# Performance work log

Measured on AMD Instinct MI355X. Metric: run time of the kernel, lower is better.

## Reference

```python
import jax, jax.numpy as jnp
import numpy as np

COORD_W, WIDTH_W, CLASS_W, P0_W = 5.0, 2.0, 1.0, 2.0
BETA = 0.1  # SmoothL1 beta
PEN_W = jnp.array([0.1, 1.0, 1.0], jnp.float32)  # CE class weights


def _lsa(C):
    """Jonker-Volgenant shortest-augmenting-path LAP, equivalent to
    scipy.optimize.linear_sum_assignment (rectangular, minimization)."""
    C = np.asarray(C, np.float64)
    transposed = C.shape[1] < C.shape[0]
    if transposed:
        C = C.T
    n, m = C.shape  # n <= m
    u = np.zeros(n)
    v = np.zeros(m)
    col4row = np.full(n, -1, np.int64)
    row4col = np.full(m, -1, np.int64)
    for cur in range(n):
        shortest = np.full(m, np.inf)
        path = np.full(m, -1, np.int64)
        SC = np.zeros(m, bool)
        SR = []
        minVal = 0.0
        i = cur
        sink = -1
        while sink == -1:
            SR.append(i)
            d = minVal + C[i] - u[i] - v
            upd = (~SC) & (d < shortest)
            shortest[upd] = d[upd]
            path[upd] = i
            masked = np.where(SC, np.inf, shortest)
            j = int(np.argmin(masked))
            minVal = float(masked[j])
            SC[j] = True
            if row4col[j] < 0:
                sink = j
            else:
                i = int(row4col[j])
        u[cur] += minVal
        for r in SR:
            if r != cur:
                u[r] += minVal - shortest[col4row[r]]
        v[SC] -= minVal - shortest[SC]
        j = sink
        while True:
            i = int(path[j])
            row4col[j] = i
            nxt = int(col4row[i])
            col4row[i] = j
            if i == cur:
                break
            j = nxt
    if transposed:
        return col4row.copy(), np.arange(n)
    return np.arange(n), col4row.copy()


def _match(strokes, pen_state_logits, targets_params, targets_labels):
    """Hungarian matching (detached, host-side like the torch original).
    Returns padded index tensors usable by vectorized gathers."""
    probs = np.asarray(jax.nn.softmax(pen_state_logits, axis=-1), np.float64)
    ps = np.asarray(strokes, np.float64)
    tp = np.asarray(targets_params, np.float64)
    tl = np.asarray(targets_labels)
    B, S, _ = ps.shape
    G = tl.shape[1]
    tc = np.zeros((B, S), np.int32)        # target class per slot (0 = null)
    pidx = np.zeros((B, G), np.int32)      # matched pred slot indices (padded)
    gidx = np.zeros((B, G), np.int32)      # matched gt indices (padded)
    mask = np.zeros((B, G), np.float32)    # 1 where a real match exists
    for b in range(B):
        valid = np.where(tl[b] > 0)[0]
        nv = valid.size
        if nv == 0:
            continue
        vt = tp[b, valid]                       # [nv, 10]
        gt_cls = tl[b, valid]                   # [nv]
        cost_class = -probs[b][:, gt_cls]       # [S, nv]
        cost_coord = np.abs(ps[b][:, None, :8] - vt[None, :, :8]).sum(-1)
        cost_width = np.abs(ps[b][:, None, 8:10] - vt[None, :, 8:10]).sum(-1)
        cost_p0 = np.abs(ps[b][:, None, :2] - vt[None, :, :2]).sum(-1)
        C = CLASS_W * cost_class + COORD_W * cost_coord + WIDTH_W * cost_width + P0_W * cost_p0
        r, c = _lsa(C)
        og = valid[c]
        tc[b, r] = tl[b, og]
        k = r.size
        pidx[b, :k] = r
        gidx[b, :k] = og
        mask[b, :k] = 1.0
    return jnp.asarray(tc), jnp.asarray(pidx), jnp.asarray(gidx), jnp.asarray(mask)


def _loss(strokes, pen_state_logits, targets_params, tc, pidx, gidx, mask):
    # Weighted cross-entropy (torch CrossEntropyLoss with class weights, mean).
    logp = jax.nn.log_softmax(pen_state_logits, axis=-1)          # [B,S,3]
    nll = -jnp.take_along_axis(logp, tc[..., None], axis=-1)[..., 0]
    w = PEN_W[tc]
    loss_ce = (w * nll).sum() / w.sum()
    mp = jnp.take_along_axis(strokes, pidx[..., None], axis=1)        # [B,G,10]
    mg = jnp.take_along_axis(targets_params, gidx[..., None], axis=1)  # [B,G,10]
    d = mp - mg
    m = mask[..., None]
    ad8 = jnp.abs(d[..., :8])
    l1 = (ad8 * m).sum()
    sl1 = jnp.where(ad8 < BETA, 0.5 * ad8 * ad8 / BETA, ad8 - 0.5 * BETA)
    sl1 = (sl1 * m).sum()
    denom = jnp.maximum(mask.sum(), 1.0)
    loss_coord = (l1 + sl1) / denom
    loss_width = (jnp.abs(d[..., 8:10]) * m).sum() / denom
    return CLASS_W * loss_ce + COORD_W * loss_coord + WIDTH_W * loss_width


def setup_inputs() -> dict:
    key = jax.random.key(0)
    k1, k2, k3, k4 = jax.random.split(key, 4)
    B, S, G = 128, 300, 100
    strokes = jax.random.uniform(k1, (B, S, 10), dtype=jnp.float32)
    pen_state_logits = jax.random.normal(k2, (B, S, 3), dtype=jnp.float32)
    targets_params = jax.random.uniform(k3, (B, G, 10), dtype=jnp.float32)
    targets_labels = jax.random.randint(k4, (B, G), 0, 3)
    return {"strokes": strokes, "pen_state_logits": pen_state_logits,
            "targets_params": targets_params, "targets_labels": targets_labels}


def reference(strokes, pen_state_logits, targets_params, targets_labels):
    tc, pidx, gidx, mask = _match(strokes, pen_state_logits, targets_params, targets_labels)
    return _loss(strokes, pen_state_logits, targets_params, tc, pidx, gidx, mask)
```

## Files before the change

kernel.cpp:

```cpp
#include <hip/hip_runtime.h>
#include <math.h>
#include <stdint.h>

#define NB 128
#define NS 300
#define NG 100
#define NP 10
#define NSLOT 5

#define WS_ACC     0
#define WS_ROWMIN  1024
#define WS_ROWARG  103424
#define WS_DCE     154624
#define WS_BASECE  769024
#define WS_C       770048
#define WS_NEEDED  (WS_C + (size_t)NB * NG * NS * 8)

#define GET_SLOT(arr, slot, out) do { switch (slot) { \
  case 0: out = arr[0]; break; case 1: out = arr[1]; break; \
  case 2: out = arr[2]; break; case 3: out = arr[3]; break; \
  default: out = arr[4]; break; } } while (0)
#define SET_SLOT(arr, slot, val) do { switch (slot) { \
  case 0: arr[0] = val; break; case 1: arr[1] = val; break; \
  case 2: arr[2] = val; break; case 3: arr[3] = val; break; \
  default: arr[4] = val; break; } } while (0)

__device__ __forceinline__ double wave_sum(double v) {
  #pragma unroll
  for (int off = 32; off > 0; off >>= 1) v += __shfl_xor(v, off);
  return v;
}

__device__ __forceinline__ uint64_t pack_key(double d) {
  const uint64_t b = (uint64_t)__double_as_longlong(d);
  return (b >> 63) ? ~b : (b | 0x8000000000000000ull);
}
__device__ __forceinline__ double unpack_key(uint64_t k) {
  const uint64_t b = (k >> 63) ? (k & 0x7fffffffffffffffull) : ~k;
  return __longlong_as_double((long long)b);
}

__device__ __forceinline__ double rl_f64(double v, int src) {
  const uint64_t b = (uint64_t)__double_as_longlong(v);
  const int lo = __builtin_amdgcn_readlane((int)(uint32_t)b, src);
  const int hi = __builtin_amdgcn_readlane((int)(uint32_t)(b >> 32), src);
  return __longlong_as_double((long long)(((uint64_t)(uint32_t)hi << 32) |
                                          (uint32_t)lo));
}

template <int CTRL>
__device__ __forceinline__ uint64_t dpp_u64_or_max(uint64_t x) {
  const int lo = (int)(uint32_t)x;
  const int hi = (int)(uint32_t)(x >> 32);
  const int lo2 = __builtin_amdgcn_update_dpp(-1, lo, CTRL, 0xF, 0xF, false);
  const int hi2 = __builtin_amdgcn_update_dpp(-1, hi, CTRL, 0xF, 0xF, false);
  return ((uint64_t)(uint32_t)hi2 << 32) | (uint32_t)lo2;
}

__device__ __forceinline__ void wave_argmin(uint64_t key, int bestj,
                                            double& minVal, int& jstar) {
  uint64_t k = key;
  { const uint64_t o = dpp_u64_or_max<0x111>(k); if (o < k) k = o; }
  { const uint64_t o = dpp_u64_or_max<0x112>(k); if (o < k) k = o; }
  { const uint64_t o = dpp_u64_or_max<0x114>(k); if (o < k) k = o; }
  { const uint64_t o = dpp_u64_or_max<0x118>(k); if (o < k) k = o; }
  { const uint64_t o = dpp_u64_or_max<0x142>(k); if (o < k) k = o; }
  { const uint64_t o = dpp_u64_or_max<0x143>(k); if (o < k) k = o; }
  const uint32_t mlo = (uint32_t)__builtin_amdgcn_readlane((int)(uint32_t)k, 63);
  const uint32_t mhi = (uint32_t)__builtin_amdgcn_readlane((int)(uint32_t)(k >> 32), 63);
  const uint64_t minkey = ((uint64_t)mhi << 32) | mlo;
  const unsigned long long winners = __ballot(key == minkey);
  const int src = __ffsll(winners) - 1;
  jstar = __builtin_amdgcn_readlane(bestj, src);
  minVal = unpack_key(minkey);
}

__device__ __forceinline__ int argmin32_src(double bestv) {
  const uint64_t key = pack_key(bestv);
  const uint32_t hi = (uint32_t)(key >> 32);
  int x = (int)hi;
  { const int o = __builtin_amdgcn_update_dpp(-1, x, 0x111, 0xF, 0xF, false);
    x = ((uint32_t)o < (uint32_t)x) ? o : x; }
  { const int o = __builtin_amdgcn_update_dpp(-1, x, 0x112, 0xF, 0xF, false);
    x = ((uint32_t)o < (uint32_t)x) ? o : x; }
  { const int o = __builtin_amdgcn_update_dpp(-1, x, 0x114, 0xF, 0xF, false);
    x = ((uint32_t)o < (uint32_t)x) ? o : x; }
  { const int o = __builtin_amdgcn_update_dpp(-1, x, 0x118, 0xF, 0xF, false);
    x = ((uint32_t)o < (uint32_t)x) ? o : x; }
  { const int o = __builtin_amdgcn_update_dpp(-1, x, 0x142, 0xF, 0xF, false);
    x = ((uint32_t)o < (uint32_t)x) ? o : x; }
  { const int o = __builtin_amdgcn_update_dpp(-1, x, 0x143, 0xF, 0xF, false);
    x = ((uint32_t)o < (uint32_t)x) ? o : x; }
  const uint32_t minhi = (uint32_t)__builtin_amdgcn_readlane(x, 63);
  unsigned long long cand = __ballot(hi == minhi);
  int src = __ffsll(cand) - 1;
  if (__popcll(cand) > 1) {
    uint64_t bk = ~0ull; int bs = src;
    while (cand) {
      const int l = __ffsll(cand) - 1; cand &= cand - 1;
      const uint32_t klo = (uint32_t)__builtin_amdgcn_readlane((int)(uint32_t)key, l);
      const uint32_t khi = (uint32_t)__builtin_amdgcn_readlane((int)(uint32_t)(key >> 32), l);
      const uint64_t kk = ((uint64_t)khi << 32) | klo;
      if (kk < bk) { bk = kk; bs = l; }
    }
    src = bs;
  }
  return src;
}

__global__ __launch_bounds__(256) void detr_cost_kernel(
    const float* __restrict__ strokes,
    const float* __restrict__ logits,
    const float* __restrict__ tparams,
    const int*   __restrict__ tlabels,
    double*      __restrict__ C,
    double*      __restrict__ dce,
    double*      __restrict__ baseCE,
    double*      __restrict__ rowmin,
    int*         __restrict__ rowarg)
{
  __shared__ float  sS[NS * NP];
  __shared__ float  sP[NS * 3];
  __shared__ float  sVT[10 * NP];
  __shared__ int    sCls[10];
  __shared__ int    s_valid[NG];
  __shared__ int    s_vlab[NG];
  __shared__ int    s_nv;
  __shared__ double s_bp[4];
  __shared__ double sC[10 * NS];

  const int b   = blockIdx.x;
  const int cb  = blockIdx.y;
  const int tid = threadIdx.x;

  for (int idx = tid; idx < NS * NP; idx += 256)
    sS[idx] = strokes[b * NS * NP + idx];

  for (int j = tid; j < NS; j += 256) {
    const float x0 = logits[(b * NS + j) * 3 + 0];
    const float x1 = logits[(b * NS + j) * 3 + 1];
    const float x2 = logits[(b * NS + j) * 3 + 2];
    const float m  = fmaxf(x0, fmaxf(x1, x2));
    const float e0 = expf(x0 - m), e1 = expf(x1 - m), e2 = expf(x2 - m);
    const float s  = e0 + e1 + e2;
    sP[j * 3 + 0] = e0 / s;
    sP[j * 3 + 1] = e1 / s;
    sP[j * 3 + 2] = e2 / s;
  }

  if (tid < 64) {
    const unsigned long long below = (1ull << tid) - 1ull;
    const int lb1 = tlabels[b * NG + tid];
    const bool in2 = tid < (NG - 64);
    const int lb2 = in2 ? tlabels[b * NG + 64 + tid] : 0;
    const unsigned long long m1 = __ballot(lb1 > 0);
    const unsigned long long m2 = __ballot(in2 && lb2 > 0);
    const int c1 = __popcll(m1);
    if (lb1 > 0) {
      const int p = __popcll(m1 & below);
      s_valid[p] = tid; s_vlab[p] = lb1;
    }
    if (in2 && lb2 > 0) {
      const int p = c1 + __popcll(m2 & below);
      s_valid[p] = 64 + tid; s_vlab[p] = lb2;
    }
    if (tid == 0) s_nv = c1 + __popcll(m2);
  }
  __syncthreads();

  if (cb == 0) {
    double bsum = 0.0;
    for (int s = tid; s < NS; s += 256) {
      const double x0 = (double)logits[(b * NS + s) * 3 + 0];
      const double x1 = (double)logits[(b * NS + s) * 3 + 1];
      const double x2 = (double)logits[(b * NS + s) * 3 + 2];
      const double m   = fmax(x0, fmax(x1, x2));
      const double lse = log(exp(x0 - m) + exp(x1 - m) + exp(x2 - m));
      const double nll0 = -(x0 - m - lse);
      const double nll1 = -(x1 - m - lse);
      const double nll2 = -(x2 - m - lse);
      dce[((size_t)b * NS + s) * 2 + 0] = nll1 - 0.1 * nll0;
      dce[((size_t)b * NS + s) * 2 + 1] = nll2 - 0.1 * nll0;
      bsum += 0.1 * nll0;
    }
    bsum = wave_sum(bsum);
    if ((tid & 63) == 0) s_bp[tid >> 6] = bsum;
    __syncthreads();
    if (tid == 0) baseCE[b] = (s_bp[0] + s_bp[1]) + (s_bp[2] + s_bp[3]);
  }

  const int nv = s_nv;
  const int i0 = cb * 10;
  const int nrow = (nv - i0 < 10) ? (nv - i0) : 10;
  if (nrow <= 0) return;

  for (int idx = tid; idx < nrow * NP; idx += 256) {
    const int il = idx / NP, k = idx % NP;
    sVT[il * NP + k] = tparams[(b * NG + s_valid[i0 + il]) * NP + k];
  }
  if (tid < nrow) sCls[tid] = s_vlab[i0 + tid];
  __syncthreads();

  for (int e = tid; e < nrow * NS; e += 256) {
    const int il = e / NS, j = e - il * NS;
    const int cls = sCls[il];
    const double p = (double)sP[j * 3 + cls];
    double a[NP];
    #pragma unroll
    for (int k = 0; k < NP; ++k)
      a[k] = fabs((double)sS[j * NP + k] - (double)sVT[il * NP + k]);
    const double coord = ((a[0] + a[1]) + (a[2] + a[3])) +
                         ((a[4] + a[5]) + (a[6] + a[7]));
    const double c = -p + 5.0 * coord + 2.0 * (a[8] + a[9]) +
                     2.0 * (a[0] + a[1]);
    C[((size_t)b * NG + (i0 + il)) * NS + j] = c;
    sC[il * NS + j] = c;
  }
  __syncthreads();

  const int wid  = tid >> 6;
  const int lane = tid & 63;
  const int vmask = (lane < NS - 4 * 64) ? 0x1F : 0x0F;
  for (int row = wid; row < nrow; row += 4) {
    double bestv = (double)INFINITY;
    int    bestj = 0x7fffffff;
    #pragma unroll
    for (int s = 0; s < NSLOT; ++s) {
      if ((vmask >> s) & 1) {
        const double c = sC[row * NS + lane + 64 * s];
        if (c < bestv) { bestv = c; bestj = lane + 64 * s; }
      }
    }
    double mv; int js;
    wave_argmin(pack_key(bestv), bestj, mv, js);
    if (lane == 0) {
      rowmin[b * NG + i0 + row] = mv;
      rowarg[b * NG + i0 + row] = js;
    }
  }
}

__global__ __launch_bounds__(64) void detr_match_fast_kernel(
    const float*  __restrict__ strokes,
    const float*  __restrict__ tparams,
    const int*    __restrict__ tlabels,
    const double* __restrict__ C,
    const double* __restrict__ rowmin,
    const int*    __restrict__ rowarg,
    const double* __restrict__ dce,
    const double* __restrict__ baseCE,
    double*       __restrict__ acc)
{
  __shared__ int    s_valid[NG];
  __shared__ int    s_vlab[NG];
  __shared__ int    s_col4row[NG];
  __shared__ int    s_claimC[NS];
  __shared__ int    s_r4cL[NS];
  __shared__ double s_short[NS];

  const int b    = blockIdx.x;
  const int lane = threadIdx.x;

  for (int j = lane; j < NS; j += 64) {
    s_claimC[j] = 0x7fffffff; s_r4cL[j] = -1;
  }

  const unsigned long long below = (1ull << lane) - 1ull;
  const int lb1 = tlabels[b * NG + lane];
  const bool in2 = lane < (NG - 64);
  const int lb2 = in2 ? tlabels[b * NG + 64 + lane] : 0;
  const unsigned long long m1 = __ballot(lb1 > 0);
  const unsigned long long m2 = __ballot(in2 && lb2 > 0);
  const int c1 = __popcll(m1);
  if (lb1 > 0) {
    const int p = __popcll(m1 & below);
    s_valid[p] = lane; s_vlab[p] = lb1;
  }
  if (in2 && lb2 > 0) {
    const int p = c1 + __popcll(m2 & below);
    s_valid[p] = 64 + lane; s_vlab[p] = lb2;
  }
  const int nv = c1 + __popcll(m2);

  for (int i = lane; i < nv; i += 64) s_col4row[i] = -1;
  __syncthreads();

  double wnll = 0.0;

  if (nv > 0) {
    const double* Cb = C + (size_t)b * NG * NS;
    const double INF = (double)INFINITY;
    const int vmask = (lane < NS - 4 * 64) ? 0x1F : 0x0F;

    double rm0 = 0.0, rm1 = 0.0;
    int    ra0 = -1,  ra1 = -1;
    if (lane < nv) {
      rm0 = rowmin[b * NG + lane];
      ra0 = rowarg[b * NG + lane];
    }
    if (lane + 64 < nv) {
      rm1 = rowmin[b * NG + lane + 64];
      ra1 = rowarg[b * NG + lane + 64];
    }

    if (lane < nv)      atomicMin(&s_claimC[ra0], lane);
    if (lane + 64 < nv) atomicMin(&s_claimC[ra1], lane + 64);
    __syncthreads();
    if (lane < nv && s_claimC[ra0] == lane) {
      s_r4cL[ra0] = lane; s_col4row[lane] = ra0;
    }
    if (lane + 64 < nv && s_claimC[ra1] == lane + 64) {
      s_r4cL[ra1] = lane + 64; s_col4row[lane + 64] = ra1;
    }
    __syncthreads();

    int r4c[NSLOT];
    #pragma unroll
    for (int s = 0; s < NSLOT; ++s)
      r4c[s] = ((vmask >> s) & 1) ? s_r4cL[lane + 64 * s] : -1;
    double vv[NSLOT];
    #pragma unroll
    for (int s = 0; s < NSLOT; ++s) vv[s] = 0.0;

    double u0 = rm0, u1 = rm1;

    unsigned long long f0 = __ballot(lane < nv && s_col4row[lane] < 0);
    unsigned long long f1 = __ballot(lane + 64 < nv && s_col4row[lane + 64] < 0);

    int pf_row = -1;
    double pfv[NSLOT];
    #pragma unroll
    for (int s = 0; s < NSLOT; ++s) pfv[s] = 0.0;

#define PRELOAD(ROW) do { \
      const double* Pr_ = Cb + (size_t)(ROW) * NS; \
      pfv[0] = Pr_[lane]; \
      pfv[1] = Pr_[lane + 64]; \
      pfv[2] = Pr_[lane + 128]; \
      pfv[3] = Pr_[lane + 192]; \
      if (lane < NS - 256) pfv[4] = Pr_[lane + 256]; \
    } while (0)

    {
      int n = -1;
      if (f0) n = __ffsll(f0) - 1; else if (f1) n = 64 + __ffsll(f1) - 1;
      if (n >= 0) { pf_row = n; PRELOAD(n); }
    }

    while (f0 | f1) {
      int cur;
      if (f0) { cur = __ffsll(f0) - 1; f0 &= f0 - 1; }
      else    { cur = 64 + __ffsll(f1) - 1; f1 &= f1 - 1; }

      double sh[NSLOT];
      int    pa[NSLOT];
      #pragma unroll
      for (int s = 0; s < NSLOT; ++s) { sh[s] = INF; pa[s] = -1; }
      int scm = 0;
      unsigned long long srm0 = 0ull, srm1 = 0ull;
      double minVal = 0.0;
      int i = cur;
      int sink = -1;

      while (sink == -1) {
        if (i < 64) srm0 |= (1ull << i); else srm1 |= (1ull << (i - 64));
        const double ucur = (i < 64) ? rl_f64(u0, i) : rl_f64(u1, i - 64);
        const double base = minVal - ucur;

        double cv[NSLOT];
        if (i == pf_row) {
          #pragma unroll
          for (int s = 0; s < NSLOT; ++s) cv[s] = pfv[s];
        } else {
          const double* Gr = Cb + (size_t)i * NS;
          #pragma unroll
          for (int s = 0; s < NSLOT; ++s)
            if ((vmask >> s) & 1) cv[s] = Gr[lane + 64 * s];
        }

        double bestv = INF;
        int    bestj = 0x7fffffff;
        #pragma unroll
        for (int s = 0; s < NSLOT; ++s) {
          if ((vmask >> s) & 1) {
            if (!((scm >> s) & 1)) {
              const double dd = base + cv[s] - vv[s];
              if (dd < sh[s]) { sh[s] = dd; pa[s] = i; }
              if (sh[s] < bestv) { bestv = sh[s]; bestj = lane + 64 * s; }
            }
          }
        }

        const int src = argmin32_src(bestv);
        const int jstar = __builtin_amdgcn_readlane(bestj, src);
        minVal = rl_f64(bestv, src);
        const int slot = jstar >> 6;
        const int jl   = jstar & 63;
        if (lane == jl) scm |= (1 << slot);

        int t;
        GET_SLOT(r4c, slot, t);
        const int rc = __builtin_amdgcn_readlane(t, jl);
        if (rc < 0) {
          sink = jstar;
        } else {
          i = rc;
          double b2 = INF;
          int    bj2 = 0x7fffffff;
          #pragma unroll
          for (int s = 0; s < NSLOT; ++s) {
            if ((vmask >> s) & 1) {
              if (!((scm >> s) & 1) && sh[s] < b2) {
                b2 = sh[s]; bj2 = lane + 64 * s;
              }
            }
          }
          const int src2 = argmin32_src(b2);
          const int j2 = __builtin_amdgcn_readlane(bj2, src2);
          int t2;
          GET_SLOT(r4c, (j2 >> 6), t2);
          const int rc2 = __builtin_amdgcn_readlane(t2, j2 & 63);
          if (rc2 >= 0 && rc2 != i) { pf_row = rc2; PRELOAD(rc2); }
          else pf_row = -1;
        }
      }

      #pragma unroll
      for (int s = 0; s < NSLOT; ++s)
        if ((vmask >> s) & 1) s_short[lane + 64 * s] = sh[s];
      __syncthreads();

      if (((srm0 >> lane) & 1ull) && lane != cur)
        u0 += minVal - s_short[s_col4row[lane]];
      const int r2 = lane + 64;
      if (((srm1 >> lane) & 1ull) && r2 != cur)
        u1 += minVal - s_short[s_col4row[r2]];
      if (lane == cur) u0 += minVal;
      if (r2 == cur)   u1 += minVal;
      #pragma unroll
      for (int s = 0; s < NSLOT; ++s)
        if ((scm >> s) & 1) vv[s] -= minVal - sh[s];
      __syncthreads();

      int j = sink;
      while (true) {
        const int slot = j >> 6, src3 = j & 63;
        int t;
        GET_SLOT(pa, slot, t);
        const int i2 = __builtin_amdgcn_readlane(t, src3);
        if (lane == src3) SET_SLOT(r4c, slot, i2);
        const int nxt = s_col4row[i2];
        if (lane == 0) s_col4row[i2] = j;
        if (i2 == cur) break;
        j = nxt;
      }
      __syncthreads();

      {
        int n = -1;
        if (f0) n = __ffsll(f0) - 1; else if (f1) n = 64 + __ffsll(f1) - 1;
        if (n >= 0) { pf_row = n; PRELOAD(n); }
      }
    }
#undef PRELOAD

    double l1 = 0.0, sl1 = 0.0, wid = 0.0;
    for (int i = lane; i < nv; i += 64) {
      const int r = s_col4row[i];
      const int c = s_vlab[i];
      wnll += dce[((size_t)b * NS + r) * 2 + (c - 1)];
      const float* ps = strokes + ((size_t)b * NS + r) * NP;
      const float* tp = tparams + ((size_t)b * NG + s_valid[i]) * NP;
      #pragma unroll
      for (int k = 0; k < 8; ++k) {
        const float d  = ps[k] - tp[k];
        const float ad = fabsf(d);
        l1 += (double)ad;
        const float sm = (ad < 0.1f) ? (0.5f * ad * ad / 0.1f) : (ad - 0.05f);
        sl1 += (double)sm;
      }
      const float d8 = fabsf(ps[8] - tp[8]);
      const float d9 = fabsf(ps[9] - tp[9]);
      wid += (double)d8 + (double)d9;
    }
    l1 = wave_sum(l1); sl1 = wave_sum(sl1); wid = wave_sum(wid);
    if (lane == 0) {
      atomicAdd(&acc[2], l1);
      atomicAdd(&acc[3], sl1);
      atomicAdd(&acc[4], wid);
      atomicAdd(&acc[5], (double)nv);
    }
  }

  wnll = wave_sum(wnll);
  if (lane == 0) {
    atomicAdd(&acc[0], wnll + baseCE[b]);
    atomicAdd(&acc[1], 30.0 + 0.9 * (double)nv);
  }
}

__global__ __launch_bounds__(64) void detr_match_loss_kernel(
    const float* __restrict__ strokes,
    const float* __restrict__ logits,
    const float* __restrict__ tparams,
    const int*   __restrict__ tlabels,
    double*      __restrict__ acc)
{
  __shared__ float  s_strokes[NS * NP];
  __shared__ float  s_probs[NS * 3];
  __shared__ float  s_vt[NG * NP];
  __shared__ int    s_valid[NG];
  __shared__ int    s_vlab[NG];
  __shared__ double s_u[NG];
  __shared__ int    s_col4row[NG];
  __shared__ int    s_SRb[NG];
  __shared__ double s_shortest[NS];
  __shared__ double s_v[NS];
  __shared__ int    s_path[NS];
  __shared__ int    s_SC[NS];
  __shared__ int    s_row4col[NS];
  __shared__ int    s_tc[NS];
  __shared__ int    s_nv;

  const int b    = blockIdx.x;
  const int lane = threadIdx.x;

  for (int idx = lane; idx < NS * NP; idx += 64)
    s_strokes[idx] = strokes[b * NS * NP + idx];

  for (int j = lane; j < NS; j += 64) {
    const float x0 = logits[(b * NS + j) * 3 + 0];
    const float x1 = logits[(b * NS + j) * 3 + 1];
    const float x2 = logits[(b * NS + j) * 3 + 2];
    const float m  = fmaxf(x0, fmaxf(x1, x2));
    const float e0 = expf(x0 - m), e1 = expf(x1 - m), e2 = expf(x2 - m);
    const float s  = e0 + e1 + e2;
    s_probs[j * 3 + 0] = e0 / s;
    s_probs[j * 3 + 1] = e1 / s;
    s_probs[j * 3 + 2] = e2 / s;
    s_tc[j]      = 0;
    s_row4col[j] = -1;
    s_v[j]       = 0.0;
  }

  if (lane == 0) {
    int nv = 0;
    for (int g = 0; g < NG; ++g) {
      const int lb = tlabels[b * NG + g];
      if (lb > 0) { s_valid[nv] = g; s_vlab[nv] = lb; ++nv; }
    }
    s_nv = nv;
  }
  __syncthreads();
  const int nv = s_nv;

  for (int idx = lane; idx < nv * NP; idx += 64) {
    const int i = idx / NP, k = idx % NP;
    s_vt[idx] = tparams[(b * NG + s_valid[i]) * NP + k];
  }
  for (int i = lane; i < nv; i += 64) { s_u[i] = 0.0; s_col4row[i] = -1; }
  __syncthreads();

  if (nv > 0) {
    for (int cur = 0; cur < nv; ++cur) {
      for (int j = lane; j < NS; j += 64) {
        s_shortest[j] = 1e300;
        s_path[j]     = -1;
        s_SC[j]       = 0;
      }
      for (int r = lane; r < nv; r += 64) s_SRb[r] = 0;
      __syncthreads();

      double minVal = 0.0;
      int i = cur;
      int sink = -1;

      while (sink == -1) {
        if (lane == 0) s_SRb[i] = 1;
        const double ui  = s_u[i];
        const int    cls = s_vlab[i];
        double vtr[NP];
        #pragma unroll
        for (int k = 0; k < NP; ++k) vtr[k] = (double)s_vt[i * NP + k];
        const double base = minVal - ui;

        double bestv = 1e300;
        int    bestj = 0x7fffffff;

        for (int j = lane; j < NS; j += 64) {
          if (!s_SC[j]) {
            const double p = (double)s_probs[j * 3 + cls];
            double a[NP];
            #pragma unroll
            for (int k = 0; k < NP; ++k)
              a[k] = fabs((double)s_strokes[j * NP + k] - vtr[k]);
            const double coord = ((a[0] + a[1]) + (a[2] + a[3])) +
                                 ((a[4] + a[5]) + (a[6] + a[7]));
            const double c = -p + 5.0 * coord + 2.0 * (a[8] + a[9]) +
                             2.0 * (a[0] + a[1]);
            const double d = base + c - s_v[j];
            if (d < s_shortest[j]) { s_shortest[j] = d; s_path[j] = i; }
            const double sv = s_shortest[j];
            if (sv < bestv) { bestv = sv; bestj = j; }
          }
        }

        #pragma unroll
        for (int off = 32; off > 0; off >>= 1) {
          const double ov = __shfl_xor(bestv, off);
          const int    oj = __shfl_xor(bestj, off);
          if (ov < bestv || (ov == bestv && oj < bestj)) { bestv = ov; bestj = oj; }
        }
        minVal = bestv;
        const int jstar = bestj;
        if (lane == 0) s_SC[jstar] = 1;
        __syncthreads();
        const int rc = s_row4col[jstar];
        if (rc < 0) sink = jstar; else i = rc;
      }

      for (int r = lane; r < nv; r += 64)
        if (s_SRb[r] && r != cur)
          s_u[r] += minVal - s_shortest[s_col4row[r]];
      if (lane == 0) s_u[cur] += minVal;
      for (int j = lane; j < NS; j += 64)
        if (s_SC[j]) s_v[j] -= minVal - s_shortest[j];
      __syncthreads();

      if (lane == 0) {
        int j = sink;
        while (true) {
          const int i2 = s_path[j];
          s_row4col[j] = i2;
          const int nxt = s_col4row[i2];
          s_col4row[i2] = j;
          if (i2 == cur) break;
          j = nxt;
        }
      }
      __syncthreads();
    }

    double l1 = 0.0, sl1 = 0.0, wid = 0.0;
    for (int i = lane; i < nv; i += 64) {
      const int r = s_col4row[i];
      s_tc[r] = s_vlab[i];
      #pragma unroll
      for (int k = 0; k < 8; ++k) {
        const float d  = s_strokes[r * NP + k] - s_vt[i * NP + k];
        const float ad = fabsf(d);
        l1 += (double)ad;
        const float s = (ad < 0.1f) ? (0.5f * ad * ad / 0.1f) : (ad - 0.05f);
        sl1 += (double)s;
      }
      const float d8 = fabsf(s_strokes[r * NP + 8] - s_vt[i * NP + 8]);
      const float d9 = fabsf(s_strokes[r * NP + 9] - s_vt[i * NP + 9]);
      wid += (double)d8 + (double)d9;
    }
    l1 = wave_sum(l1); sl1 = wave_sum(sl1); wid = wave_sum(wid);
    if (lane == 0) {
      atomicAdd(&acc[2], l1);
      atomicAdd(&acc[3], sl1);
      atomicAdd(&acc[4], wid);
      atomicAdd(&acc[5], (double)nv);
    }
  }
  __syncthreads();

  double wnll = 0.0, wsum = 0.0;
  for (int s = lane; s < NS; s += 64) {
    const int tc = s_tc[s];
    const double x0 = (double)logits[(b * NS + s) * 3 + 0];
    const double x1 = (double)logits[(b * NS + s) * 3 + 1];
    const double x2 = (double)logits[(b * NS + s) * 3 + 2];
    const double m   = fmax(x0, fmax(x1, x2));
    const double lse = log(exp(x0 - m) + exp(x1 - m) + exp(x2 - m));
    const double xt  = (tc == 0) ? x0 : ((tc == 1) ? x1 : x2);
    const double nll = -(xt - m - lse);
    const double w   = (tc == 0) ? 0.1 : 1.0;
    wnll += w * nll;
    wsum += w;
  }
  wnll = wave_sum(wnll); wsum = wave_sum(wsum);
  if (lane == 0) {
    atomicAdd(&acc[0], wnll);
    atomicAdd(&acc[1], wsum);
  }
}

__global__ void detr_finalize_kernel(const double* __restrict__ acc,
                                     float* __restrict__ out) {
  const double loss_ce = acc[0] / acc[1];
  const double denom   = fmax(acc[5], 1.0);
  const double loss = 1.0 * loss_ce
                    + 5.0 * (acc[2] + acc[3]) / denom
                    + 2.0 * acc[4] / denom;
  out[0] = (float)loss;
}

extern "C" void kernel_launch(void* const* d_in, const int* in_sizes, int n_in,
                              void* d_out, int out_size, void* d_ws, size_t ws_size,
                              hipStream_t stream) {
  const float* strokes = (const float*)d_in[0];
  const float* logits  = (const float*)d_in[1];
  const float* tparams = (const float*)d_in[2];
  const int*   tlabels = (const int*)d_in[3];
  char* ws = (char*)d_ws;
  double* acc = (double*)(ws + WS_ACC);

  hipMemsetAsync(d_ws, 0, 64, stream);

  if (ws_size >= WS_NEEDED) {
    double* rowmin = (double*)(ws + WS_ROWMIN);
    int*    rowarg = (int*)(ws + WS_ROWARG);
    double* dce    = (double*)(ws + WS_DCE);
    double* baseCE = (double*)(ws + WS_BASECE);
    double* C      = (double*)(ws + WS_C);

    detr_cost_kernel<<<dim3(NB, 10), 256, 0, stream>>>(
        strokes, logits, tparams, tlabels, C, dce, baseCE, rowmin, rowarg);
    detr_match_fast_kernel<<<NB, 64, 0, stream>>>(
        strokes, tparams, tlabels, C, rowmin, rowarg, dce, baseCE, acc);
  } else {
    detr_match_loss_kernel<<<NB, 64, 0, stream>>>(strokes, logits, tparams,
                                                  tlabels, acc);
  }
  detr_finalize_kernel<<<1, 1, 0, stream>>>(acc, (float*)d_out);
}
```

Baseline: 70.85 us.

## Fuse cost-matrix build and LAP matching into one per-batch kernel with row cache

```diff
diff --git a/kernel.cpp b/kernel.cpp
--- a/kernel.cpp
+++ b/kernel.cpp
@@ -7,14 +7,11 @@
 #define NG 100
 #define NP 10
 #define NSLOT 5
-
-#define WS_ACC     0
-#define WS_ROWMIN  1024
-#define WS_ROWARG  103424
-#define WS_DCE     154624
-#define WS_BASECE  769024
-#define WS_C       770048
-#define WS_NEEDED  (WS_C + (size_t)NB * NG * NS * 8)
+#define NCROW 16
+
+#define WS_ACC 0
+#define WS_C   1024
+#define WS_NEEDED (WS_C + (size_t)NB * NG * NS * 8)
 
 #define GET_SLOT(arr, slot, out) do { switch (slot) { \
   case 0: out = arr[0]; break; case 1: out = arr[1]; break; \
@@ -108,34 +105,38 @@
   return src;
 }
 
-__global__ __launch_bounds__(256) void detr_cost_kernel(
+__global__ __launch_bounds__(256) void detr_fused_kernel(
     const float* __restrict__ strokes,
     const float* __restrict__ logits,
     const float* __restrict__ tparams,
     const int*   __restrict__ tlabels,
     double*      __restrict__ C,
-    double*      __restrict__ dce,
-    double*      __restrict__ baseCE,
-    double*      __restrict__ rowmin,
-    int*         __restrict__ rowarg)
+    double*      __restrict__ acc)
 {
   __shared__ float  sS[NS * NP];
   __shared__ float  sP[NS * 3];
-  __shared__ float  sVT[10 * NP];
-  __shared__ int    sCls[10];
   __shared__ int    s_valid[NG];
   __shared__ int    s_vlab[NG];
+  __shared__ double s_rowminL[NG];
+  __shared__ int    s_rowargL[NG];
+  __shared__ int    s_claimC[NS];
+  __shared__ int    s_r4cL[NS];
+  __shared__ double s_short[NS];
+  __shared__ int    s_col4row[NG];
+  __shared__ double s_crow[NCROW * NS];
+  __shared__ int    s_ctag[NCROW];
+  __shared__ double s_bp[4];
+  __shared__ double s_baseCE;
   __shared__ int    s_nv;
-  __shared__ double s_bp[4];
-  __shared__ double sC[10 * NS];
-
-  const int b   = blockIdx.x;
-  const int cb  = blockIdx.y;
-  const int tid = threadIdx.x;
+
+  const int b    = blockIdx.x;
+  const int tid  = threadIdx.x;
+  const int wv   = tid >> 6;
+  const int lane = tid & 63;
+  const double INF = (double)INFINITY;
 
   for (int idx = tid; idx < NS * NP; idx += 256)
     sS[idx] = strokes[b * NS * NP + idx];
-
   for (int j = tid; j < NS; j += 256) {
     const float x0 = logits[(b * NS + j) * 3 + 0];
     const float x1 = logits[(b * NS + j) * 3 + 1];
@@ -146,29 +147,34 @@
     sP[j * 3 + 0] = e0 / s;
     sP[j * 3 + 1] = e1 / s;
     sP[j * 3 + 2] = e2 / s;
-  }
+    s_claimC[j] = 0x7fffffff;
+    s_r4cL[j]   = -1;
+  }
+  if (tid < NCROW) s_ctag[tid] = -1;
 
   if (tid < 64) {
-    const unsigned long long below = (1ull << tid) - 1ull;
-    const int lb1 = tlabels[b * NG + tid];
-    const bool in2 = tid < (NG - 64);
-    const int lb2 = in2 ? tlabels[b * NG + 64 + tid] : 0;
+    const unsigned long long below = (1ull << lane) - 1ull;
+    const int lb1 = tlabels[b * NG + lane];
+    const bool in2 = lane < (NG - 64);
+    const int lb2 = in2 ? tlabels[b * NG + 64 + lane] : 0;
     const unsigned long long m1 = __ballot(lb1 > 0);
     const unsigned long long m2 = __ballot(in2 && lb2 > 0);
     const int c1 = __popcll(m1);
     if (lb1 > 0) {
       const int p = __popcll(m1 & below);
-      s_valid[p] = tid; s_vlab[p] = lb1;
+      s_valid[p] = lane; s_vlab[p] = lb1;
     }
     if (in2 && lb2 > 0) {
       const int p = c1 + __popcll(m2 & below);
-      s_valid[p] = 64 + tid; s_vlab[p] = lb2;
-    }
-    if (tid == 0) s_nv = c1 + __popcll(m2);
+      s_valid[p] = 64 + lane; s_vlab[p] = lb2;
+    }
+    if (lane == 0) s_nv = c1 + __popcll(m2);
   }
   __syncthreads();
-
-  if (cb == 0) {
+  const int nv = s_nv;
+  for (int i = tid; i < nv; i += 256) s_col4row[i] = -1;
+
+  {
     double bsum = 0.0;
     for (int s = tid; s < NS; s += 256) {
       const double x0 = (double)logits[(b * NS + s) * 3 + 0];
@@ -176,143 +182,68 @@
       const double x2 = (double)logits[(b * NS + s) * 3 + 2];
       const double m   = fmax(x0, fmax(x1, x2));
       const double lse = log(exp(x0 - m) + exp(x1 - m) + exp(x2 - m));
-      const double nll0 = -(x0 - m - lse);
-      const double nll1 = -(x1 - m - lse);
-      const double nll2 = -(x2 - m - lse);
-      dce[((size_t)b * NS + s) * 2 + 0] = nll1 - 0.1 * nll0;
-      dce[((size_t)b * NS + s) * 2 + 1] = nll2 - 0.1 * nll0;
-      bsum += 0.1 * nll0;
+      bsum += 0.1 * (-(x0 - m - lse));
     }
     bsum = wave_sum(bsum);
-    if ((tid & 63) == 0) s_bp[tid >> 6] = bsum;
-    __syncthreads();
-    if (tid == 0) baseCE[b] = (s_bp[0] + s_bp[1]) + (s_bp[2] + s_bp[3]);
-  }
-
-  const int nv = s_nv;
-  const int i0 = cb * 10;
-  const int nrow = (nv - i0 < 10) ? (nv - i0) : 10;
-  if (nrow <= 0) return;
-
-  for (int idx = tid; idx < nrow * NP; idx += 256) {
-    const int il = idx / NP, k = idx % NP;
-    sVT[il * NP + k] = tparams[(b * NG + s_valid[i0 + il]) * NP + k];
-  }
-  if (tid < nrow) sCls[tid] = s_vlab[i0 + tid];
-  __syncthreads();
-
-  for (int e = tid; e < nrow * NS; e += 256) {
-    const int il = e / NS, j = e - il * NS;
-    const int cls = sCls[il];
-    const double p = (double)sP[j * 3 + cls];
-    double a[NP];
+    if (lane == 0) s_bp[wv] = bsum;
+  }
+
+  const int vmask = (lane < NS - 4 * 64) ? 0x1F : 0x0F;
+  for (int i = wv; i < nv; i += 4) {
+    const int g   = s_valid[i];
+    const int cls = s_vlab[i];
+    double vt[NP];
     #pragma unroll
     for (int k = 0; k < NP; ++k)
-      a[k] = fabs((double)sS[j * NP + k] - (double)sVT[il * NP + k]);
-    const double coord = ((a[0] + a[1]) + (a[2] + a[3])) +
-                         ((a[4] + a[5]) + (a[6] + a[7]));
-    const double c = -p + 5.0 * coord + 2.0 * (a[8] + a[9]) +
-                     2.0 * (a[0] + a[1]);
-    C[((size_t)b * NG + (i0 + il)) * NS + j] = c;
-    sC[il * NS + j] = c;
-  }
-  __syncthreads();
-
-  const int wid  = tid >> 6;
-  const int lane = tid & 63;
-  const int vmask = (lane < NS - 4 * 64) ? 0x1F : 0x0F;
-  for (int row = wid; row < nrow; row += 4) {
-    double bestv = (double)INFINITY;
-    int    bestj = 0x7fffffff;
+      vt[k] = (double)tparams[((size_t)b * NG + g) * NP + k];
+    double cc[NSLOT];
     #pragma unroll
     for (int s = 0; s < NSLOT; ++s) {
       if ((vmask >> s) & 1) {
-        const double c = sC[row * NS + lane + 64 * s];
-        if (c < bestv) { bestv = c; bestj = lane + 64 * s; }
-      }
-    }
+        const int j = lane + 64 * s;
+        const double p = (double)sP[j * 3 + cls];
+        double a[NP];
+        #pragma unroll
+        for (int k = 0; k < NP; ++k)
+          a[k] = fabs((double)sS[j * NP + k] - vt[k]);
+        const double coord = ((a[0] + a[1]) + (a[2] + a[3])) +
+                             ((a[4] + a[5]) + (a[6] + a[7]));
+        const double c = -p + 5.0 * coord + 2.0 * (a[8] + a[9]) +
+                         2.0 * (a[0] + a[1]);
+        C[((size_t)b * NG + i) * NS + j] = c;
+        cc[s] = c;
+      } else cc[s] = INF;
+    }
+    double bestv = INF;
+    int    bestj = 0x7fffffff;
+    #pragma unroll
+    for (int s = 0; s < NSLOT; ++s)
+      if (((vmask >> s) & 1) && cc[s] < bestv) { bestv = cc[s]; bestj = lane + 64 * s; }
     double mv; int js;
     wave_argmin(pack_key(bestv), bestj, mv, js);
-    if (lane == 0) {
-      rowmin[b * NG + i0 + row] = mv;
-      rowarg[b * NG + i0 + row] = js;
-    }
-  }
-}
-
-__global__ __launch_bounds__(64) void detr_match_fast_kernel(
-    const float*  __restrict__ strokes,
-    const float*  __restrict__ tparams,
-    const int*    __restrict__ tlabels,
-    const double* __restrict__ C,
-    const double* __restrict__ rowmin,
-    const int*    __restrict__ rowarg,
-    const double* __restrict__ dce,
-    const double* __restrict__ baseCE,
-    double*       __restrict__ acc)
-{
-  __shared__ int    s_valid[NG];
-  __shared__ int    s_vlab[NG];
-  __shared__ int    s_col4row[NG];
-  __shared__ int    s_claimC[NS];
-  __shared__ int    s_r4cL[NS];
-  __shared__ double s_short[NS];
-
-  const int b    = blockIdx.x;
-  const int lane = threadIdx.x;
-
-  for (int j = lane; j < NS; j += 64) {
-    s_claimC[j] = 0x7fffffff; s_r4cL[j] = -1;
-  }
-
-  const unsigned long long below = (1ull << lane) - 1ull;
-  const int lb1 = tlabels[b * NG + lane];
-  const bool in2 = lane < (NG - 64);
-  const int lb2 = in2 ? tlabels[b * NG + 64 + lane] : 0;
-  const unsigned long long m1 = __ballot(lb1 > 0);
-  const unsigned long long m2 = __ballot(in2 && lb2 > 0);
-  const int c1 = __popcll(m1);
-  if (lb1 > 0) {
-    const int p = __popcll(m1 & below);
-    s_valid[p] = lane; s_vlab[p] = lb1;
-  }
-  if (in2 && lb2 > 0) {
-    const int p = c1 + __popcll(m2 & below);
-    s_valid[p] = 64 + lane; s_vlab[p] = lb2;
-  }
-  const int nv = c1 + __popcll(m2);
-
-  for (int i = lane; i < nv; i += 64) s_col4row[i] = -1;
+    if (lane == 0) { s_rowminL[i] = mv; s_rowargL[i] = js; }
+  }
   __syncthreads();
-
-  double wnll = 0.0;
-
-  if (nv > 0) {
+  if (tid == 0) s_baseCE = (s_bp[0] + s_bp[1]) + (s_bp[2] + s_bp[3]);
+
+  if (wv == 0 && nv > 0) {
     const double* Cb = C + (size_t)b * NG * NS;
-    const double INF = (double)INFINITY;
-    const int vmask = (lane < NS - 4 * 64) ? 0x1F : 0x0F;
 
     double rm0 = 0.0, rm1 = 0.0;
     int    ra0 = -1,  ra1 = -1;
-    if (lane < nv) {
-      rm0 = rowmin[b * NG + lane];
-      ra0 = rowarg[b * NG + lane];
-    }
-    if (lane + 64 < nv) {
-      rm1 = rowmin[b * NG + lane + 64];
-      ra1 = rowarg[b * NG + lane + 64];
-    }
+    if (lane < nv)      { rm0 = s_rowminL[lane];      ra0 = s_rowargL[lane]; }
+    if (lane + 64 < nv) { rm1 = s_rowminL[lane + 64]; ra1 = s_rowargL[lane + 64]; }
 
     if (lane < nv)      atomicMin(&s_claimC[ra0], lane);
     if (lane + 64 < nv) atomicMin(&s_claimC[ra1], lane + 64);
-    __syncthreads();
+    __builtin_amdgcn_wave_barrier();
     if (lane < nv && s_claimC[ra0] == lane) {
       s_r4cL[ra0] = lane; s_col4row[lane] = ra0;
     }
     if (lane + 64 < nv && s_claimC[ra1] == lane + 64) {
       s_r4cL[ra1] = lane + 64; s_col4row[lane + 64] = ra1;
     }
-    __syncthreads();
+    __builtin_amdgcn_wave_barrier();
 
     int r4c[NSLOT];
     #pragma unroll
@@ -367,15 +298,31 @@
         const double ucur = (i < 64) ? rl_f64(u0, i) : rl_f64(u1, i - 64);
         const double base = minVal - ucur;
 
+        const int cs = i & (NCROW - 1);
+        const bool cached = (s_ctag[cs] == i);
         double cv[NSLOT];
         if (i == pf_row) {
           #pragma unroll
           for (int s = 0; s < NSLOT; ++s) cv[s] = pfv[s];
+          if (!cached) {
+            #pragma unroll
+            for (int s = 0; s < NSLOT; ++s)
+              if ((vmask >> s) & 1) s_crow[cs * NS + lane + 64 * s] = pfv[s];
+            if (lane == 0) s_ctag[cs] = i;
+          }
+        } else if (cached) {
+          #pragma unroll
+          for (int s = 0; s < NSLOT; ++s)
+            if ((vmask >> s) & 1) cv[s] = s_crow[cs * NS + lane + 64 * s];
         } else {
           const double* Gr = Cb + (size_t)i * NS;
           #pragma unroll
           for (int s = 0; s < NSLOT; ++s)
             if ((vmask >> s) & 1) cv[s] = Gr[lane + 64 * s];
+          #pragma unroll
+          for (int s = 0; s < NSLOT; ++s)
+            if ((vmask >> s) & 1) s_crow[cs * NS + lane + 64 * s] = cv[s];
+          if (lane == 0) s_ctag[cs] = i;
         }
 
         double bestv = INF;
@@ -420,15 +367,16 @@
           int t2;
           GET_SLOT(r4c, (j2 >> 6), t2);
           const int rc2 = __builtin_amdgcn_readlane(t2, j2 & 63);
-          if (rc2 >= 0 && rc2 != i) { pf_row = rc2; PRELOAD(rc2); }
-          else pf_row = -1;
+          if (rc2 >= 0 && rc2 != i && s_ctag[rc2 & (NCROW - 1)] != rc2) {
+            pf_row = rc2; PRELOAD(rc2);
+          } else pf_row = -1;
         }
       }
 
       #pragma unroll
       for (int s = 0; s < NSLOT; ++s)
         if ((vmask >> s) & 1) s_short[lane + 64 * s] = sh[s];
-      __syncthreads();
+      __builtin_amdgcn_wave_barrier();
 
       if (((srm0 >> lane) & 1ull) && lane != cur)
         u0 += minVal - s_short[s_col4row[lane]];
@@ -440,7 +388,7 @@
       #pragma unroll
       for (int s = 0; s < NSLOT; ++s)
         if ((scm >> s) & 1) vv[s] -= minVal - sh[s];
-      __syncthreads();
+      __builtin_amdgcn_wave_barrier();
 
       int j = sink;
       while (true) {
@@ -454,7 +402,7 @@
         if (i2 == cur) break;
         j = nxt;
       }
-      __syncthreads();
+      __builtin_amdgcn_wave_barrier();
 
       {
         int n = -1;
@@ -463,39 +411,47 @@
       }
     }
 #undef PRELOAD
-
-    double l1 = 0.0, sl1 = 0.0, wid = 0.0;
-    for (int i = lane; i < nv; i += 64) {
-      const int r = s_col4row[i];
-      const int c = s_vlab[i];
-      wnll += dce[((size_t)b * NS + r) * 2 + (c - 1)];
-      const float* ps = strokes + ((size_t)b * NS + r) * NP;
-      const float* tp = tparams + ((size_t)b * NG + s_valid[i]) * NP;
-      #pragma unroll
-      for (int k = 0; k < 8; ++k) {
-        const float d  = ps[k] - tp[k];
-        const float ad = fabsf(d);
-        l1 += (double)ad;
-        const float sm = (ad < 0.1f) ? (0.5f * ad * ad / 0.1f) : (ad - 0.05f);
-        sl1 += (double)sm;
-      }
-      const float d8 = fabsf(ps[8] - tp[8]);
-      const float d9 = fabsf(ps[9] - tp[9]);
-      wid += (double)d8 + (double)d9;
-    }
-    l1 = wave_sum(l1); sl1 = wave_sum(sl1); wid = wave_sum(wid);
-    if (lane == 0) {
-      atomicAdd(&acc[2], l1);
-      atomicAdd(&acc[3], sl1);
-      atomicAdd(&acc[4], wid);
-      atomicAdd(&acc[5], (double)nv);
-    }
-  }
-
-  wnll = wave_sum(wnll);
+  }
+  __syncthreads();
+
+  double l1 = 0.0, sl1 = 0.0, wd = 0.0, wnll = 0.0;
+  for (int i = tid; i < nv; i += 256) {
+    const int r = s_col4row[i];
+    const int c = s_vlab[i];
+    {
+      const double x0 = (double)logits[(b * NS + r) * 3 + 0];
+      const double x1 = (double)logits[(b * NS + r) * 3 + 1];
+      const double x2 = (double)logits[(b * NS + r) * 3 + 2];
+      const double m   = fmax(x0, fmax(x1, x2));
+      const double lse = log(exp(x0 - m) + exp(x1 - m) + exp(x2 - m));
+      const double nll0 = -(x0 - m - lse);
+      const double nllc = -(((c == 1) ? x1 : x2) - m - lse);
+      wnll += nllc - 0.1 * nll0;
+    }
+    const float* tp = tparams + ((size_t)b * NG + s_valid[i]) * NP;
+    #pragma unroll
+    for (int k = 0; k < 8; ++k) {
+      const float d  = sS[r * NP + k] - tp[k];
+      const float ad = fabsf(d);
+      l1 += (double)ad;
+      const float sm = (ad < 0.1f) ? (0.5f * ad * ad / 0.1f) : (ad - 0.05f);
+      sl1 += (double)sm;
+    }
+    const float d8 = fabsf(sS[r * NP + 8] - tp[8]);
+    const float d9 = fabsf(sS[r * NP + 9] - tp[9]);
+    wd += (double)d8 + (double)d9;
+  }
+  l1 = wave_sum(l1); sl1 = wave_sum(sl1); wd = wave_sum(wd); wnll = wave_sum(wnll);
   if (lane == 0) {
-    atomicAdd(&acc[0], wnll + baseCE[b]);
+    atomicAdd(&acc[0], wnll);
+    atomicAdd(&acc[2], l1);
+    atomicAdd(&acc[3], sl1);
+    atomicAdd(&acc[4], wd);
+  }
+  if (tid == 0) {
+    atomicAdd(&acc[0], s_baseCE);
     atomicAdd(&acc[1], 30.0 + 0.9 * (double)nv);
+    atomicAdd(&acc[5], (double)nv);
   }
 }
 
@@ -711,16 +667,9 @@
   hipMemsetAsync(d_ws, 0, 64, stream);
 
   if (ws_size >= WS_NEEDED) {
-    double* rowmin = (double*)(ws + WS_ROWMIN);
-    int*    rowarg = (int*)(ws + WS_ROWARG);
-    double* dce    = (double*)(ws + WS_DCE);
-    double* baseCE = (double*)(ws + WS_BASECE);
-    double* C      = (double*)(ws + WS_C);
-
-    detr_cost_kernel<<<dim3(NB, 10), 256, 0, stream>>>(
-        strokes, logits, tparams, tlabels, C, dce, baseCE, rowmin, rowarg);
-    detr_match_fast_kernel<<<NB, 64, 0, stream>>>(
-        strokes, tparams, tlabels, C, rowmin, rowarg, dce, baseCE, acc);
+    double* C = (double*)(ws + WS_C);
+    detr_fused_kernel<<<NB, 256, 0, stream>>>(strokes, logits, tparams,
+                                              tlabels, C, acc);
   } else {
     detr_match_loss_kernel<<<NB, 64, 0, stream>>>(strokes, logits, tparams,
                                                   tlabels, acc);
```

After: 77.86 us. 1.1x slower.
